# Optimization experiments

Measured on AMD Instinct MI355X. Metric: run time of the kernel, lower is better.

## Reference

```python
import jax, jax.numpy as jnp
import numpy as np

B, T, E, H, V = 64, 160, 512, 1024, 32000


def setup_inputs() -> dict:
    key = jax.random.key(0)
    ks = jax.random.split(key, 8)
    s = 1.0 / np.sqrt(H).astype(np.float32)
    return {
        "contexts": jax.random.randint(ks[0], (B, T), 0, V),
        "responses": jax.random.randint(ks[1], (B, T), 0, V),
        "emb": jax.random.normal(ks[2], (V, E), jnp.float32) * 0.02,
        "Wih": jax.random.uniform(ks[3], (4 * H, E), jnp.float32, -s, s),
        "Whh": jax.random.uniform(ks[4], (4 * H, H), jnp.float32, -s, s),
        "bih": jax.random.uniform(ks[5], (4 * H,), jnp.float32, -s, s),
        "bhh": jax.random.uniform(ks[6], (4 * H,), jnp.float32, -s, s),
        "M": jax.random.normal(ks[7], (H, H), jnp.float32),
    }


def _lstm_final_h(tokens, emb, Wih, Whh, bih, bhh):
    """Single-layer LSTM (PyTorch gate order i,f,g,o); returns final hidden state [B,H]."""
    x = emb[tokens]                      # [B, T, E]
    b = bih + bhh                        # [4H]
    hdim = Whh.shape[1]

    def step(carry, xt):
        h, c = carry
        gates = xt @ Wih.T + h @ Whh.T + b          # [B, 4H]
        i, f, g, o = jnp.split(gates, 4, axis=-1)
        c = jax.nn.sigmoid(f) * c + jax.nn.sigmoid(i) * jnp.tanh(g)
        h = jax.nn.sigmoid(o) * jnp.tanh(c)
        return (h, c), None

    h0 = jnp.zeros((tokens.shape[0], hdim), x.dtype)
    (h, _), _ = jax.lax.scan(step, (h0, h0), jnp.swapaxes(x, 0, 1))  # scan over time
    return h


def reference(contexts, responses, emb, Wih, Whh, bih, bhh, M):
    ch = _lstm_final_h(contexts, emb, Wih, Whh, bih, bhh)   # [B, H]
    rh = _lstm_final_h(responses, emb, Wih, Whh, bih, bhh)  # [B, H]
    # batched bilinear: sigmoid(diag(C @ M @ R^T)) -- replaces the per-example Python loop
    return jax.nn.sigmoid(jnp.einsum('bi,ij,bj->b', ch, M, rh))
```

## Files before the change

### kernel.cpp

```cpp
#include <hip/hip_runtime.h>
#include <math.h>


#define BB 64
#define TT 160
#define EE 512
#define HH 1024
#define G4 4096
#define ROWS 128

typedef unsigned short u16;
typedef __attribute__((ext_vector_type(8))) __bf16 bf16x8;
typedef __attribute__((ext_vector_type(8))) short short8;
typedef __attribute__((ext_vector_type(4))) short short4v;
typedef __attribute__((ext_vector_type(4))) float f32x4;

__device__ inline u16 f2b(float f) {
    unsigned u = __float_as_uint(f);
    u = u + 0x7fffu + ((u >> 16) & 1u);
    return (u16)(u >> 16);
}
__device__ inline float b2f(u16 s) { return __uint_as_float(((unsigned)s) << 16); }

__device__ inline f32x4 mfma16(const u16* a, const u16* b, f32x4 c) {
    bf16x8 av = __builtin_bit_cast(bf16x8, *(const short8*)a);
    bf16x8 bv = __builtin_bit_cast(bf16x8, *(const short8*)b);
    return __builtin_amdgcn_mfma_f32_16x16x32_bf16(av, bv, c, 0, 0, 0);
}

__global__ __launch_bounds__(256) void cvt_kernel(const float* __restrict__ in,
                                                  u16* __restrict__ out, int n4) {
    int i = blockIdx.x * 256 + threadIdx.x;
    if (i < n4) {
        f32x4 v = *(const f32x4*)(in + (size_t)i * 4);
        short4v o;
        o.x = (short)f2b(v.x); o.y = (short)f2b(v.y);
        o.z = (short)f2b(v.z); o.w = (short)f2b(v.w);
        *(short4v*)(out + (size_t)i * 4) = o;
    }
}

__global__ __launch_bounds__(256) void pre_gemm(
    const int* __restrict__ ctx, const int* __restrict__ rsp,
    const u16* __restrict__ embb, const u16* __restrict__ Wihb,
    const float* __restrict__ bih, const float* __restrict__ bhh,
    u16* __restrict__ xg)
{
    __shared__ __align__(16) u16 As[128][32];
    __shared__ __align__(16) u16 Ws[128][32];
    __shared__ int toks[128];
    const int tid = threadIdx.x;
    const int n0 = blockIdx.x * 128;
    const int t  = blockIdx.y;

    if (tid < 128) {
        int r = tid;
        toks[tid] = (r < BB) ? ctx[r * TT + t] : rsp[(r - BB) * TT + t];
    }
    __syncthreads();

    const int lane = tid & 63, wave = tid >> 6;
    const int wr = (wave >> 1) * 64, wc = (wave & 1) * 64;
    const int l15 = lane & 15, l4 = lane >> 4;

    f32x4 acc[4][4] = {};

    for (int it = 0; it < 16; ++it) {
        const int kg = it * 32;
        #pragma unroll
        for (int half = 0; half < 2; ++half) {
            int cc = tid + half * 256;
            int row = cc >> 2, seg = (cc & 3) * 8;
            *(short8*)&As[row][seg] = *(const short8*)(embb + (size_t)toks[row] * EE + kg + seg);
            *(short8*)&Ws[row][seg] = *(const short8*)(Wihb + (size_t)(n0 + row) * EE + kg + seg);
        }
        __syncthreads();
        #pragma unroll
        for (int mf = 0; mf < 4; ++mf)
            #pragma unroll
            for (int nf = 0; nf < 4; ++nf)
                acc[mf][nf] = mfma16(&As[wr + mf * 16 + l15][l4 * 8],
                                     &Ws[wc + nf * 16 + l15][l4 * 8], acc[mf][nf]);
        __syncthreads();
    }

    u16* xp = xg + (size_t)t * ROWS * G4;
    #pragma unroll
    for (int mf = 0; mf < 4; ++mf)
        #pragma unroll
        for (int nf = 0; nf < 4; ++nf) {
            int n = n0 + wc + nf * 16 + l15;
            float bias = bih[n] + bhh[n];
            #pragma unroll
            for (int q = 0; q < 4; ++q) {
                int r = wr + mf * 16 + l4 * 4 + q;
                xp[(size_t)r * G4 + n] = f2b(acc[mf][nf][q] + bias);
            }
        }
}

template<bool CONV, bool XPRE>
__global__ __launch_bounds__(256) void step_gemm(
    const int* __restrict__ ctx, const int* __restrict__ rsp,
    const float* __restrict__ emb, const float* __restrict__ Wih, const float* __restrict__ Whh,
    const u16* __restrict__ embb, const u16* __restrict__ Wihb, const u16* __restrict__ Whhb,
    const u16* __restrict__ hb, float* __restrict__ gates, int t)
{
    __shared__ __align__(16) u16 As[64][32];
    __shared__ __align__(16) u16 Ws[64][32];
    __shared__ int toks[64];

    const int tid = threadIdx.x;
    const int n0 = blockIdx.x * 64;
    const int r0 = blockIdx.y * 64;
    const int part = blockIdx.z;

    if (!XPRE) {
        if (tid < 64) {
            int r = r0 + tid;
            toks[tid] = (r < BB) ? ctx[r * TT + t] : rsp[(r - BB) * TT + t];
        }
        __syncthreads();
    }

    const int lane = tid & 63, wave = tid >> 6;
    const int wr = (wave >> 1) * 32, wc = (wave & 1) * 32;
    const int l15 = lane & 15, l4 = lane >> 4;

    f32x4 acc[2][2] = {};

    const int kstart = XPRE ? (EE + part * 512) : part * 768;
    const int niter  = XPRE ? 16 : 24;

    const int srow = tid >> 2;
    const int sseg = (tid & 3) * 8;

    for (int it = 0; it < niter; ++it) {
        const int kg = kstart + it * 32;
        const int kk = kg + sseg;
        if (!XPRE && kg < EE) {
            int tok = toks[srow];
            if (CONV) {
                const float* s = emb + (size_t)tok * EE + kk;
                #pragma unroll
                for (int q = 0; q < 8; ++q) As[srow][sseg + q] = f2b(s[q]);
            } else {
                *(short8*)&As[srow][sseg] = *(const short8*)(embb + (size_t)tok * EE + kk);
            }
        } else {
            *(short8*)&As[srow][sseg] = *(const short8*)(hb + (size_t)(r0 + srow) * HH + (kk - EE));
        }
        {
            int ng = n0 + srow;
            if (!XPRE && kg < EE) {
                if (CONV) {
                    const float* s = Wih + (size_t)ng * EE + kk;
                    #pragma unroll
                    for (int q = 0; q < 8; ++q) Ws[srow][sseg + q] = f2b(s[q]);
                } else {
                    *(short8*)&Ws[srow][sseg] = *(const short8*)(Wihb + (size_t)ng * EE + kk);
                }
            } else {
                if (CONV) {
                    const float* s = Whh + (size_t)ng * HH + (kk - EE);
                    #pragma unroll
                    for (int q = 0; q < 8; ++q) Ws[srow][sseg + q] = f2b(s[q]);
                } else {
                    *(short8*)&Ws[srow][sseg] = *(const short8*)(Whhb + (size_t)ng * HH + (kk - EE));
                }
            }
        }
        __syncthreads();
        #pragma unroll
        for (int mf = 0; mf < 2; ++mf)
            #pragma unroll
            for (int nf = 0; nf < 2; ++nf)
                acc[mf][nf] = mfma16(&As[wr + mf * 16 + l15][l4 * 8],
                                     &Ws[wc + nf * 16 + l15][l4 * 8], acc[mf][nf]);
        __syncthreads();
    }

    float* gp = gates + (size_t)part * ROWS * G4;
    #pragma unroll
    for (int mf = 0; mf < 2; ++mf)
        #pragma unroll
        for (int nf = 0; nf < 2; ++nf)
            #pragma unroll
            for (int q = 0; q < 4; ++q) {
                int r = r0 + wr + mf * 16 + l4 * 4 + q;
                int n = n0 + wc + nf * 16 + l15;
                gp[(size_t)r * G4 + n] = acc[mf][nf][q];
            }
}

template<bool XPRE>
__global__ __launch_bounds__(256) void lstm_update(
    const float* __restrict__ gates, const u16* __restrict__ xg,
    const float* __restrict__ bih, const float* __restrict__ bhh,
    u16* __restrict__ hb, float* __restrict__ c, int t)
{
    int idx = blockIdx.x * 256 + threadIdx.x;
    int r = idx >> 8;
    int jj = (idx & 255) * 4;
    const float* g0 = gates + (size_t)r * G4;
    const float* g1 = gates + (size_t)(ROWS + r) * G4;
    float gate[4][4];
    #pragma unroll
    for (int g = 0; g < 4; ++g) {
        int n = g * HH + jj;
        f32x4 a = *(const f32x4*)(g0 + n);
        f32x4 b = *(const f32x4*)(g1 + n);
        #pragma unroll
        for (int q = 0; q < 4; ++q) gate[g][q] = a[q] + b[q];
        if (XPRE) {
            const u16* xp = xg + ((size_t)t * ROWS + r) * G4 + n;
            #pragma unroll
            for (int q = 0; q < 4; ++q) gate[g][q] += b2f(xp[q]);
        } else {
            #pragma unroll
            for (int q = 0; q < 4; ++q) gate[g][q] += bih[n + q] + bhh[n + q];
        }
    }
    int cidx = r * HH + jj;
    f32x4 cv = *(const f32x4*)(c + cidx);
    f32x4 cn;
    short4v hn;
    #pragma unroll
    for (int q = 0; q < 4; ++q) {
        float si = 1.f / (1.f + expf(-gate[0][q]));
        float sf = 1.f / (1.f + expf(-gate[1][q]));
        float tg = tanhf(gate[2][q]);
        float so = 1.f / (1.f + expf(-gate[3][q]));
        float cval = sf * cv[q] + si * tg;
        cn[q] = cval;
        float hval = so * tanhf(cval);
        ((short*)&hn)[q] = (short)f2b(hval);
    }
    *(f32x4*)(c + cidx) = cn;
    *(short4v*)(hb + cidx) = hn;
}

__global__ __launch_bounds__(256) void bilinear(
    const u16* __restrict__ hb, const float* __restrict__ M, float* __restrict__ out)
{
    int b = blockIdx.x;
    __shared__ float chs[HH];
    __shared__ float red[256];
    const u16* ch = hb + (size_t)b * HH;
    const u16* rh = hb + (size_t)(BB + b) * HH;
    for (int i = threadIdx.x; i < HH; i += 256) chs[i] = b2f(ch[i]);
    __syncthreads();
    float vj[4] = {0.f, 0.f, 0.f, 0.f};
    for (int i = 0; i < HH; ++i) {
        float chi = chs[i];
        const float* Mr = M + (size_t)i * HH;
        #pragma unroll
        for (int q = 0; q < 4; ++q) vj[q] += chi * Mr[threadIdx.x + q * 256];
    }
    float acc = 0.f;
    #pragma unroll
    for (int q = 0; q < 4; ++q) acc += vj[q] * b2f(rh[threadIdx.x + q * 256]);
    red[threadIdx.x] = acc;
    __syncthreads();
    for (int s = 128; s > 0; s >>= 1) {
        if (threadIdx.x < s) red[threadIdx.x] += red[threadIdx.x + s];
        __syncthreads();
    }
    if (threadIdx.x == 0) out[b] = 1.0f / (1.0f + expf(-red[0]));
}

extern "C" void kernel_launch(void* const* d_in, const int* in_sizes, int n_in,
                              void* d_out, int out_size, void* d_ws, size_t ws_size,
                              hipStream_t stream) {
    const int*   ctx = (const int*)d_in[0];
    const int*   rsp = (const int*)d_in[1];
    const float* emb = (const float*)d_in[2];
    const float* Wih = (const float*)d_in[3];
    const float* Whh = (const float*)d_in[4];
    const float* bih = (const float*)d_in[5];
    const float* bhh = (const float*)d_in[6];
    const float* M   = (const float*)d_in[7];
    float* out = (float*)d_out;

    char* w = (char*)d_ws;
    u16*   hb    = (u16*)w;   w += (size_t)ROWS * HH * 2;
    float* c     = (float*)w; w += (size_t)ROWS * HH * 4;
    float* gates = (float*)w; w += (size_t)2 * ROWS * G4 * 4;
    size_t base_need = (size_t)(w - (char*)d_ws);
    u16*   embb  = (u16*)w;   w += (size_t)32000 * EE * 2;
    u16*   Wihb  = (u16*)w;   w += (size_t)G4 * EE * 2;
    u16*   Whhb  = (u16*)w;   w += (size_t)G4 * HH * 2;
    size_t conv_need = (size_t)(w - (char*)d_ws);
    u16*   xg    = (u16*)w;   w += (size_t)TT * ROWS * G4 * 2;
    size_t xpre_need = (size_t)(w - (char*)d_ws);

    int mode = (ws_size >= xpre_need) ? 2 : (ws_size >= conv_need) ? 1 : 0;
    (void)base_need;

    hipMemsetAsync(hb, 0, (size_t)ROWS * HH * 2, stream);
    hipMemsetAsync(c,  0, (size_t)ROWS * HH * 4, stream);

    if (mode >= 1) {
        cvt_kernel<<<16000, 256, 0, stream>>>(emb, embb, 32000 * EE / 4);
        cvt_kernel<<<2048,  256, 0, stream>>>(Wih, Wihb, G4 * EE / 4);
        cvt_kernel<<<4096,  256, 0, stream>>>(Whh, Whhb, G4 * HH / 4);
    }
    if (mode == 2) {
        pre_gemm<<<dim3(G4 / 128, TT), 256, 0, stream>>>(ctx, rsp, embb, Wihb, bih, bhh, xg);
    }

    dim3 sg(G4 / 64, ROWS / 64, 2);
    for (int t = 0; t < TT; ++t) {
        if (mode == 2)
            step_gemm<false, true><<<sg, 256, 0, stream>>>(ctx, rsp, emb, Wih, Whh,
                embb, Wihb, Whhb, hb, gates, t);
        else if (mode == 1)
            step_gemm<false, false><<<sg, 256, 0, stream>>>(ctx, rsp, emb, Wih, Whh,
                embb, Wihb, Whhb, hb, gates, t);
        else
            step_gemm<true, false><<<sg, 256, 0, stream>>>(ctx, rsp, emb, Wih, Whh,
                embb, Wihb, Whhb, hb, gates, t);
        if (mode == 2)
            lstm_update<true><<<128, 256, 0, stream>>>(gates, xg, bih, bhh, hb, c, t);
        else
            lstm_update<false><<<128, 256, 0, stream>>>(gates, xg, bih, bhh, hb, c, t);
    }
    bilinear<<<BB, 256, 0, stream>>>(hb, M, out);
}
```

Measured before the change: 2.344 ms.

## Fuse recurrent GEMM with LSTM cell update and pipeline LDS loads via global_load_lds

```diff
diff --git a/kernel.cpp b/kernel.cpp
--- a/kernel.cpp
+++ b/kernel.cpp
@@ -10,22 +10,28 @@
 #define ROWS 128
 
 typedef unsigned short u16;
+typedef unsigned int u32;
 typedef __attribute__((ext_vector_type(8))) __bf16 bf16x8;
 typedef __attribute__((ext_vector_type(8))) short short8;
 typedef __attribute__((ext_vector_type(4))) short short4v;
 typedef __attribute__((ext_vector_type(4))) float f32x4;
 
-__device__ inline u16 f2b(float f) {
+__device__ __forceinline__ u16 f2b(float f) {
     unsigned u = __float_as_uint(f);
     u = u + 0x7fffu + ((u >> 16) & 1u);
     return (u16)(u >> 16);
 }
-__device__ inline float b2f(u16 s) { return __uint_as_float(((unsigned)s) << 16); }
-
-__device__ inline f32x4 mfma16(const u16* a, const u16* b, f32x4 c) {
-    bf16x8 av = __builtin_bit_cast(bf16x8, *(const short8*)a);
-    bf16x8 bv = __builtin_bit_cast(bf16x8, *(const short8*)b);
-    return __builtin_amdgcn_mfma_f32_16x16x32_bf16(av, bv, c, 0, 0, 0);
+__device__ __forceinline__ float b2f(u16 s) { return __uint_as_float(((unsigned)s) << 16); }
+
+__device__ __forceinline__ f32x4 mfma16(short8 a, short8 b, f32x4 c) {
+    return __builtin_amdgcn_mfma_f32_16x16x32_bf16(
+        __builtin_bit_cast(bf16x8, a), __builtin_bit_cast(bf16x8, b), c, 0, 0, 0);
+}
+
+__device__ __forceinline__ void g2l16(const void* gsrc, void* ldst) {
+    __builtin_amdgcn_global_load_lds(
+        (const __attribute__((address_space(1))) u32*)gsrc,
+        (__attribute__((address_space(3))) u32*)ldst, 16, 0, 0);
 }
 
 __global__ __launch_bounds__(256) void cvt_kernel(const float* __restrict__ in,
@@ -40,14 +46,14 @@
     }
 }
 
-__global__ __launch_bounds__(256) void pre_gemm(
+__global__ __launch_bounds__(256) void pre_gemm2(
     const int* __restrict__ ctx, const int* __restrict__ rsp,
     const u16* __restrict__ embb, const u16* __restrict__ Wihb,
     const float* __restrict__ bih, const float* __restrict__ bhh,
     u16* __restrict__ xg)
 {
-    __shared__ __align__(16) u16 As[128][32];
-    __shared__ __align__(16) u16 Ws[128][32];
+    __shared__ __align__(16) u16 As[2][128][64];
+    __shared__ __align__(16) u16 Ws[2][128][64];
     __shared__ int toks[128];
     const int tid = threadIdx.x;
     const int n0 = blockIdx.x * 128;
@@ -59,127 +65,245 @@
     }
     __syncthreads();
 
+    const u16* asrc[4]; const u16* bsrc[4];
+    #pragma unroll
+    for (int q = 0; q < 4; ++q) {
+        int i = tid + q * 256;
+        int row = i >> 3, c16 = i & 7;
+        int scol = ((c16 ^ (row & 7)) * 8);
+        asrc[q] = embb + (size_t)toks[row] * EE + scol;
+        bsrc[q] = Wihb + (size_t)(n0 + row) * EE + scol;
+    }
+
     const int lane = tid & 63, wave = tid >> 6;
     const int wr = (wave >> 1) * 64, wc = (wave & 1) * 64;
     const int l15 = lane & 15, l4 = lane >> 4;
-
     f32x4 acc[4][4] = {};
 
-    for (int it = 0; it < 16; ++it) {
-        const int kg = it * 32;
-        #pragma unroll
-        for (int half = 0; half < 2; ++half) {
-            int cc = tid + half * 256;
-            int row = cc >> 2, seg = (cc & 3) * 8;
-            *(short8*)&As[row][seg] = *(const short8*)(embb + (size_t)toks[row] * EE + kg + seg);
-            *(short8*)&Ws[row][seg] = *(const short8*)(Wihb + (size_t)(n0 + row) * EE + kg + seg);
-        }
-        __syncthreads();
+    #pragma unroll
+    for (int q = 0; q < 4; ++q) {
+        g2l16(asrc[q], (char*)&As[0][0][0] + (tid + q * 256) * 16);
+        g2l16(bsrc[q], (char*)&Ws[0][0][0] + (tid + q * 256) * 16);
+    }
+    for (int it = 0; it < 8; ++it) {
+        __syncthreads();
+        if (it + 1 < 8) {
+            int kk = (it + 1) * 64, bs = (it + 1) & 1;
+            #pragma unroll
+            for (int q = 0; q < 4; ++q) {
+                g2l16(asrc[q] + kk, (char*)&As[bs][0][0] + (tid + q * 256) * 16);
+                g2l16(bsrc[q] + kk, (char*)&Ws[bs][0][0] + (tid + q * 256) * 16);
+            }
+        }
+        const int b = it & 1;
+        #pragma unroll
+        for (int ks = 0; ks < 2; ++ks) {
+            int c16 = ks * 4 + l4;
+            short8 a[4], w[4];
+            #pragma unroll
+            for (int mf = 0; mf < 4; ++mf) {
+                int R = wr + mf * 16 + l15;
+                a[mf] = *(const short8*)((const char*)&As[b][0][0] + R * 128 + ((c16 ^ (R & 7)) << 4));
+            }
+            #pragma unroll
+            for (int nf = 0; nf < 4; ++nf) {
+                int Nn = wc + nf * 16 + l15;
+                w[nf] = *(const short8*)((const char*)&Ws[b][0][0] + Nn * 128 + ((c16 ^ (Nn & 7)) << 4));
+            }
+            #pragma unroll
+            for (int mf = 0; mf < 4; ++mf)
+                #pragma unroll
+                for (int nf = 0; nf < 4; ++nf)
+                    acc[mf][nf] = mfma16(a[mf], w[nf], acc[mf][nf]);
+        }
+    }
+
+    u16* xp = xg + (size_t)t * ROWS * G4;
+    #pragma unroll
+    for (int nf = 0; nf < 4; ++nf) {
+        int n = n0 + wc + nf * 16 + l15;
+        float bias = bih[n] + bhh[n];
         #pragma unroll
         for (int mf = 0; mf < 4; ++mf)
-            #pragma unroll
-            for (int nf = 0; nf < 4; ++nf)
-                acc[mf][nf] = mfma16(&As[wr + mf * 16 + l15][l4 * 8],
-                                     &Ws[wc + nf * 16 + l15][l4 * 8], acc[mf][nf]);
-        __syncthreads();
-    }
-
-    u16* xp = xg + (size_t)t * ROWS * G4;
-    #pragma unroll
-    for (int mf = 0; mf < 4; ++mf)
-        #pragma unroll
-        for (int nf = 0; nf < 4; ++nf) {
-            int n = n0 + wc + nf * 16 + l15;
-            float bias = bih[n] + bhh[n];
             #pragma unroll
             for (int q = 0; q < 4; ++q) {
                 int r = wr + mf * 16 + l4 * 4 + q;
                 xp[(size_t)r * G4 + n] = f2b(acc[mf][nf][q] + bias);
             }
-        }
-}
-
-template<bool CONV, bool XPRE>
-__global__ __launch_bounds__(256) void step_gemm(
+    }
+}
+
+template<int MODE>
+__global__ __launch_bounds__(256) void step_fused(
+    const int* __restrict__ ctx, const int* __restrict__ rsp,
+    const u16* __restrict__ embb, const u16* __restrict__ Wihb,
+    const u16* __restrict__ Whhb, const u16* __restrict__ xg,
+    const float* __restrict__ bih, const float* __restrict__ bhh,
+    const u16* __restrict__ hin, u16* __restrict__ hout,
+    float* __restrict__ c_ws, int t)
+{
+    __shared__ __align__(16) u16 As[2][64][64];
+    __shared__ __align__(16) u16 Ws[2][32][64];
+    __shared__ float gs[64][32];
+    __shared__ int toks[64];
+
+    const int tid = threadIdx.x;
+    const int cg = blockIdx.x & 127, rg = blockIdx.x >> 7;
+    const int r0 = rg * 64, j0 = cg * 8;
+
+    if (MODE == 1) {
+        if (tid < 64) {
+            int r = r0 + tid;
+            toks[tid] = (r < BB) ? ctx[r * TT + t] : rsp[(r - BB) * TT + t];
+        }
+        __syncthreads();
+    }
+
+    const int arow0 = tid >> 3, c16a = tid & 7;
+    const int arow1 = arow0 + 32;
+    const int acol0 = ((c16a ^ (arow0 & 7)) * 8);
+    const int acol1 = ((c16a ^ (arow1 & 7)) * 8);
+    const u16* hA0 = hin + (size_t)(r0 + arow0) * HH + acol0;
+    const u16* hA1 = hin + (size_t)(r0 + arow1) * HH + acol1;
+    const u16* eA0 = nullptr; const u16* eA1 = nullptr;
+    if (MODE == 1) {
+        eA0 = embb + (size_t)toks[arow0] * EE + acol0;
+        eA1 = embb + (size_t)toks[arow1] * EE + acol1;
+    }
+    const int nn = tid >> 3, c16b = tid & 7;
+    const int bcol = ((c16b ^ (nn & 7)) * 8);
+    const int wrow = (nn >> 3) * HH + j0 + (nn & 7);
+    const u16* wHh = Whhb + (size_t)wrow * HH + bcol;
+    const u16* wIh = (MODE == 1) ? (Wihb + (size_t)wrow * EE + bcol) : nullptr;
+
+    const int NK = (MODE == 1) ? 24 : 16;
+
+    auto stage = [&](int bs, int it) {
+        int kk = it * 64;
+        const u16 *s0, *s1, *sw;
+        if (MODE == 1 && kk < EE) {
+            s0 = eA0 + kk; s1 = eA1 + kk; sw = wIh + kk;
+        } else {
+            int kh = (MODE == 1) ? kk - EE : kk;
+            s0 = hA0 + kh; s1 = hA1 + kh; sw = wHh + kh;
+        }
+        g2l16(s0, (char*)&As[bs][0][0] + tid * 16);
+        g2l16(s1, (char*)&As[bs][0][0] + (tid + 256) * 16);
+        g2l16(sw, (char*)&Ws[bs][0][0] + tid * 16);
+    };
+
+    const int lane = tid & 63, wave = tid >> 6;
+    const int wr = wave * 16;
+    const int l15 = lane & 15, l4 = lane >> 4;
+    f32x4 acc[2] = {};
+
+    stage(0, 0);
+    for (int it = 0; it < NK; ++it) {
+        __syncthreads();
+        if (it + 1 < NK) stage((it + 1) & 1, it + 1);
+        const int b = it & 1;
+        #pragma unroll
+        for (int ks = 0; ks < 2; ++ks) {
+            int c16 = ks * 4 + l4;
+            int R = wr + l15;
+            short8 a = *(const short8*)((const char*)&As[b][0][0] + R * 128 + ((c16 ^ (R & 7)) << 4));
+            #pragma unroll
+            for (int nf = 0; nf < 2; ++nf) {
+                int Nn = nf * 16 + l15;
+                short8 w = *(const short8*)((const char*)&Ws[b][0][0] + Nn * 128 + ((c16 ^ (Nn & 7)) << 4));
+                acc[nf] = mfma16(a, w, acc[nf]);
+            }
+        }
+    }
+    __syncthreads();
+    #pragma unroll
+    for (int nf = 0; nf < 2; ++nf)
+        #pragma unroll
+        for (int q = 0; q < 4; ++q)
+            gs[wr + l4 * 4 + q][nf * 16 + l15] = acc[nf][q];
+    __syncthreads();
+
+    const int e = tid * 2;
+    const int row = e >> 3, jj = e & 7;
+    const int rglob = r0 + row;
+    float g0[4], g1[4];
+    #pragma unroll
+    for (int g = 0; g < 4; ++g) { g0[g] = gs[row][g * 8 + jj]; g1[g] = gs[row][g * 8 + jj + 1]; }
+    if (MODE == 2) {
+        const u16* xp = xg + ((size_t)t * ROWS + rglob) * G4 + j0 + jj;
+        #pragma unroll
+        for (int g = 0; g < 4; ++g) { g0[g] += b2f(xp[g * HH]); g1[g] += b2f(xp[g * HH + 1]); }
+    } else {
+        #pragma unroll
+        for (int g = 0; g < 4; ++g) {
+            int n = g * HH + j0 + jj;
+            g0[g] += bih[n] + bhh[n];
+            g1[g] += bih[n + 1] + bhh[n + 1];
+        }
+    }
+    size_t cidx = ((size_t)blockIdx.x * 64 + row) * 8 + jj;
+    float c0 = c_ws[cidx], c1 = c_ws[cidx + 1];
+    float i0 = 1.f / (1.f + expf(-g0[0])), i1 = 1.f / (1.f + expf(-g1[0]));
+    float f0 = 1.f / (1.f + expf(-g0[1])), f1 = 1.f / (1.f + expf(-g1[1]));
+    float t0 = tanhf(g0[2]),               t1 = tanhf(g1[2]);
+    float o0 = 1.f / (1.f + expf(-g0[3])), o1 = 1.f / (1.f + expf(-g1[3]));
+    float cn0 = f0 * c0 + i0 * t0;
+    float cn1 = f1 * c1 + i1 * t1;
+    c_ws[cidx] = cn0; c_ws[cidx + 1] = cn1;
+    float h0 = o0 * tanhf(cn0), h1 = o1 * tanhf(cn1);
+    unsigned hp = (unsigned)f2b(h0) | ((unsigned)f2b(h1) << 16);
+    *(unsigned*)(hout + (size_t)rglob * HH + j0 + jj) = hp;
+}
+
+__global__ __launch_bounds__(256) void step_gemm_f32(
     const int* __restrict__ ctx, const int* __restrict__ rsp,
     const float* __restrict__ emb, const float* __restrict__ Wih, const float* __restrict__ Whh,
-    const u16* __restrict__ embb, const u16* __restrict__ Wihb, const u16* __restrict__ Whhb,
     const u16* __restrict__ hb, float* __restrict__ gates, int t)
 {
     __shared__ __align__(16) u16 As[64][32];
     __shared__ __align__(16) u16 Ws[64][32];
     __shared__ int toks[64];
-
     const int tid = threadIdx.x;
     const int n0 = blockIdx.x * 64;
     const int r0 = blockIdx.y * 64;
     const int part = blockIdx.z;
-
-    if (!XPRE) {
-        if (tid < 64) {
-            int r = r0 + tid;
-            toks[tid] = (r < BB) ? ctx[r * TT + t] : rsp[(r - BB) * TT + t];
-        }
-        __syncthreads();
-    }
-
+    if (tid < 64) {
+        int r = r0 + tid;
+        toks[tid] = (r < BB) ? ctx[r * TT + t] : rsp[(r - BB) * TT + t];
+    }
+    __syncthreads();
     const int lane = tid & 63, wave = tid >> 6;
     const int wr = (wave >> 1) * 32, wc = (wave & 1) * 32;
     const int l15 = lane & 15, l4 = lane >> 4;
-
     f32x4 acc[2][2] = {};
-
-    const int kstart = XPRE ? (EE + part * 512) : part * 768;
-    const int niter  = XPRE ? 16 : 24;
-
+    const int kstart = part * 768;
     const int srow = tid >> 2;
     const int sseg = (tid & 3) * 8;
-
-    for (int it = 0; it < niter; ++it) {
+    for (int it = 0; it < 24; ++it) {
         const int kg = kstart + it * 32;
         const int kk = kg + sseg;
-        if (!XPRE && kg < EE) {
-            int tok = toks[srow];
-            if (CONV) {
-                const float* s = emb + (size_t)tok * EE + kk;
-                #pragma unroll
-                for (int q = 0; q < 8; ++q) As[srow][sseg + q] = f2b(s[q]);
-            } else {
-                *(short8*)&As[srow][sseg] = *(const short8*)(embb + (size_t)tok * EE + kk);
-            }
+        if (kg < EE) {
+            const float* s = emb + (size_t)toks[srow] * EE + kk;
+            #pragma unroll
+            for (int q = 0; q < 8; ++q) As[srow][sseg + q] = f2b(s[q]);
+            const float* sw = Wih + (size_t)(n0 + srow) * EE + kk;
+            #pragma unroll
+            for (int q = 0; q < 8; ++q) Ws[srow][sseg + q] = f2b(sw[q]);
         } else {
             *(short8*)&As[srow][sseg] = *(const short8*)(hb + (size_t)(r0 + srow) * HH + (kk - EE));
-        }
-        {
-            int ng = n0 + srow;
-            if (!XPRE && kg < EE) {
-                if (CONV) {
-                    const float* s = Wih + (size_t)ng * EE + kk;
-                    #pragma unroll
-                    for (int q = 0; q < 8; ++q) Ws[srow][sseg + q] = f2b(s[q]);
-                } else {
-                    *(short8*)&Ws[srow][sseg] = *(const short8*)(Wihb + (size_t)ng * EE + kk);
-                }
-            } else {
-                if (CONV) {
-                    const float* s = Whh + (size_t)ng * HH + (kk - EE);
-                    #pragma unroll
-                    for (int q = 0; q < 8; ++q) Ws[srow][sseg + q] = f2b(s[q]);
-                } else {
-                    *(short8*)&Ws[srow][sseg] = *(const short8*)(Whhb + (size_t)ng * HH + (kk - EE));
-                }
-            }
+            const float* sw = Whh + (size_t)(n0 + srow) * HH + (kk - EE);
+            #pragma unroll
+            for (int q = 0; q < 8; ++q) Ws[srow][sseg + q] = f2b(sw[q]);
         }
         __syncthreads();
         #pragma unroll
         for (int mf = 0; mf < 2; ++mf)
             #pragma unroll
             for (int nf = 0; nf < 2; ++nf)
-                acc[mf][nf] = mfma16(&As[wr + mf * 16 + l15][l4 * 8],
-                                     &Ws[wc + nf * 16 + l15][l4 * 8], acc[mf][nf]);
-        __syncthreads();
-    }
-
+                acc[mf][nf] = mfma16(*(const short8*)&As[wr + mf * 16 + l15][l4 * 8],
+                                     *(const short8*)&Ws[wc + nf * 16 + l15][l4 * 8], acc[mf][nf]);
+        __syncthreads();
+    }
     float* gp = gates + (size_t)part * ROWS * G4;
     #pragma unroll
     for (int mf = 0; mf < 2; ++mf)
@@ -193,38 +317,27 @@
             }
 }
 
-template<bool XPRE>
-__global__ __launch_bounds__(256) void lstm_update(
-    const float* __restrict__ gates, const u16* __restrict__ xg,
-    const float* __restrict__ bih, const float* __restrict__ bhh,
-    u16* __restrict__ hb, float* __restrict__ c, int t)
+__global__ __launch_bounds__(256) void lstm_update0(
+    const float* __restrict__ gates, const float* __restrict__ bih, const float* __restrict__ bhh,
+    u16* __restrict__ hb, float* __restrict__ c)
 {
     int idx = blockIdx.x * 256 + threadIdx.x;
     int r = idx >> 8;
     int jj = (idx & 255) * 4;
-    const float* g0 = gates + (size_t)r * G4;
-    const float* g1 = gates + (size_t)(ROWS + r) * G4;
+    const float* gp0 = gates + (size_t)r * G4;
+    const float* gp1 = gates + (size_t)(ROWS + r) * G4;
     float gate[4][4];
     #pragma unroll
     for (int g = 0; g < 4; ++g) {
         int n = g * HH + jj;
-        f32x4 a = *(const f32x4*)(g0 + n);
-        f32x4 b = *(const f32x4*)(g1 + n);
-        #pragma unroll
-        for (int q = 0; q < 4; ++q) gate[g][q] = a[q] + b[q];
-        if (XPRE) {
-            const u16* xp = xg + ((size_t)t * ROWS + r) * G4 + n;
-            #pragma unroll
-            for (int q = 0; q < 4; ++q) gate[g][q] += b2f(xp[q]);
-        } else {
-            #pragma unroll
-            for (int q = 0; q < 4; ++q) gate[g][q] += bih[n + q] + bhh[n + q];
-        }
+        f32x4 a = *(const f32x4*)(gp0 + n);
+        f32x4 b = *(const f32x4*)(gp1 + n);
+        #pragma unroll
+        for (int q = 0; q < 4; ++q) gate[g][q] = a[q] + b[q] + bih[n + q] + bhh[n + q];
     }
     int cidx = r * HH + jj;
     f32x4 cv = *(const f32x4*)(c + cidx);
-    f32x4 cn;
-    short4v hn;
+    f32x4 cn; short4v hn;
     #pragma unroll
     for (int q = 0; q < 4; ++q) {
         float si = 1.f / (1.f + expf(-gate[0][q]));
@@ -233,8 +346,7 @@
         float so = 1.f / (1.f + expf(-gate[3][q]));
         float cval = sf * cv[q] + si * tg;
         cn[q] = cval;
-        float hval = so * tanhf(cval);
-        ((short*)&hn)[q] = (short)f2b(hval);
+        ((short*)&hn)[q] = (short)f2b(so * tanhf(cval));
     }
     *(f32x4*)(c + cidx) = cn;
     *(short4v*)(hb + cidx) = hn;
@@ -283,10 +395,9 @@
     float* out = (float*)d_out;
 
     char* w = (char*)d_ws;
-    u16*   hb    = (u16*)w;   w += (size_t)ROWS * HH * 2;
-    float* c     = (float*)w; w += (size_t)ROWS * HH * 4;
+    u16*   hbuf  = (u16*)w;   w += (size_t)2 * ROWS * HH * 2;
+    float* c_ws  = (float*)w; w += (size_t)ROWS * HH * 4;
     float* gates = (float*)w; w += (size_t)2 * ROWS * G4 * 4;
-    size_t base_need = (size_t)(w - (char*)d_ws);
     u16*   embb  = (u16*)w;   w += (size_t)32000 * EE * 2;
     u16*   Wihb  = (u16*)w;   w += (size_t)G4 * EE * 2;
     u16*   Whhb  = (u16*)w;   w += (size_t)G4 * HH * 2;
@@ -295,35 +406,38 @@
     size_t xpre_need = (size_t)(w - (char*)d_ws);
 
     int mode = (ws_size >= xpre_need) ? 2 : (ws_size >= conv_need) ? 1 : 0;
-    (void)base_need;
-
-    hipMemsetAsync(hb, 0, (size_t)ROWS * HH * 2, stream);
-    hipMemsetAsync(c,  0, (size_t)ROWS * HH * 4, stream);
+
+    hipMemsetAsync(hbuf, 0, (size_t)2 * ROWS * HH * 2, stream);
+    hipMemsetAsync(c_ws, 0, (size_t)ROWS * HH * 4, stream);
 
     if (mode >= 1) {
         cvt_kernel<<<16000, 256, 0, stream>>>(emb, embb, 32000 * EE / 4);
         cvt_kernel<<<2048,  256, 0, stream>>>(Wih, Wihb, G4 * EE / 4);
         cvt_kernel<<<4096,  256, 0, stream>>>(Whh, Whhb, G4 * HH / 4);
     }
-    if (mode == 2) {
-        pre_gemm<<<dim3(G4 / 128, TT), 256, 0, stream>>>(ctx, rsp, embb, Wihb, bih, bhh, xg);
-    }
-
-    dim3 sg(G4 / 64, ROWS / 64, 2);
-    for (int t = 0; t < TT; ++t) {
-        if (mode == 2)
-            step_gemm<false, true><<<sg, 256, 0, stream>>>(ctx, rsp, emb, Wih, Whh,
-                embb, Wihb, Whhb, hb, gates, t);
-        else if (mode == 1)
-            step_gemm<false, false><<<sg, 256, 0, stream>>>(ctx, rsp, emb, Wih, Whh,
-                embb, Wihb, Whhb, hb, gates, t);
-        else
-            step_gemm<true, false><<<sg, 256, 0, stream>>>(ctx, rsp, emb, Wih, Whh,
-                embb, Wihb, Whhb, hb, gates, t);
-        if (mode == 2)
-            lstm_update<true><<<128, 256, 0, stream>>>(gates, xg, bih, bhh, hb, c, t);
-        else
-            lstm_update<false><<<128, 256, 0, stream>>>(gates, xg, bih, bhh, hb, c, t);
-    }
-    bilinear<<<BB, 256, 0, stream>>>(hb, M, out);
-}
+    if (mode == 2)
+        pre_gemm2<<<dim3(G4 / 128, TT), 256, 0, stream>>>(ctx, rsp, embb, Wihb, bih, bhh, xg);
+
+    if (mode >= 1) {
+        for (int t = 0; t < TT; ++t) {
+            const u16* hin = hbuf + (size_t)(t & 1) * ROWS * HH;
+            u16* hout      = hbuf + (size_t)((t + 1) & 1) * ROWS * HH;
+            if (mode == 2)
+                step_fused<2><<<256, 256, 0, stream>>>(ctx, rsp, embb, Wihb, Whhb, xg,
+                                                       bih, bhh, hin, hout, c_ws, t);
+            else
+                step_fused<1><<<256, 256, 0, stream>>>(ctx, rsp, embb, Wihb, Whhb, xg,
+                                                       bih, bhh, hin, hout, c_ws, t);
+        }
+        bilinear<<<BB, 256, 0, stream>>>(hbuf, M, out);
+    } else {
+        u16* hb = hbuf;
+        float* c = c_ws;
+        dim3 sg(G4 / 64, ROWS / 64, 2);
+        for (int t = 0; t < TT; ++t) {
+            step_gemm_f32<<<sg, 256, 0, stream>>>(ctx, rsp, emb, Wih, Whh, hb, gates, t);
+            lstm_update0<<<128, 256, 0, stream>>>(gates, bih, bhh, hb, c);
+        }
+        bilinear<<<BB, 256, 0, stream>>>(hb, M, out);
+    }
+}
```

Measured after the change: 2.164 ms. 1.08x faster.
